# Kernel optimization log

Measured on AMD Instinct MI355X. Metric: run time of the kernel, lower is better.

The kernel has to match this reference:

```python
import jax, jax.numpy as jnp
import numpy as np

N, P = 512, 256
GAMMA = 1.0


def _linear_w(key, out_dim, in_dim):
    # torch nn.Linear default init: U(-1/sqrt(fan_in), 1/sqrt(fan_in))
    bound = 1.0 / np.sqrt(in_dim)
    return jax.random.uniform(key, (out_dim, in_dim), jnp.float32, -bound, bound)


def setup_inputs() -> dict:
    key = jax.random.key(0)
    ks = jax.random.split(key, 11)
    grad = jax.random.normal(ks[0], (N, P), jnp.float32)
    gradm1 = jax.random.normal(ks[1], (N, P), jnp.float32)
    dm1 = jax.random.normal(ks[2], (N, P), jnp.float32)
    # reset_mat(n_traj=N): identity per trajectory
    predicted_mat = jnp.broadcast_to(jnp.eye(P, dtype=jnp.float32), (N, P, P)).copy()
    return {
        "grad": grad, "gradm1": gradm1, "dm1": dm1, "predicted_mat": predicted_mat,
        "W_fullskip": _linear_w(ks[3], 1, 6),
        "Wo1": _linear_w(ks[4], 6, 3),
        "Wo2": _linear_w(ks[5], 12, 6),
        "Wo3": _linear_w(ks[6], 3, 12),
        "Wl1": _linear_w(ks[7], 12, 6),
        "Wl2": _linear_w(ks[8], 24, 12),
        "Wl3": _linear_w(ks[9], 1, 24),
    }


def reference(grad, gradm1, dm1, predicted_mat, W_fullskip, Wo1, Wo2, Wo3, Wl1, Wl2, Wl3):
    relu = jax.nn.relu
    # --- construct_features (torch.no_grad) ---
    QNDG = jnp.einsum('npq,nq->np', predicted_mat, grad - gradm1)          # (N,P)
    Bg = -GAMMA * jnp.einsum('npq,nq->np', predicted_mat, grad)            # (N,P)
    # cat along feature dim then reshape(N,3,P).transpose -> stack on last axis
    x = jnp.stack([QNDG, dm1, Bg], axis=-1)                                # (N,P,3)
    x = jax.lax.stop_gradient(x)
    # --- outer_FF: per-coordinate tiny MLP, then mean over P ---
    of = relu(x @ Wo1.T)
    of = relu(of @ Wo2.T)
    of = of @ Wo3.T                                                        # (N,P,3)
    of = jnp.mean(of, axis=1)                                              # (N,3)
    of = jnp.broadcast_to(of[:, None, :], x.shape)                         # (N,P,3)
    x6 = jnp.concatenate([x, of], axis=-1)                                 # (N,P,6)
    # --- full skip connection ---
    fullskip = (x6 @ W_fullskip.T)[..., 0]                                 # (N,P)
    # --- inner MLP (layers) ---
    out = relu(x6 @ Wl1.T)
    out = relu(out @ Wl2.T)
    out = (out @ Wl3.T)[..., 0]                                            # (N,P)
    out = out + fullskip
    # --- BFGS-like rank-2 update ---
    DGK = grad - gradm1                                                    # (N,P)
    secant = x[:, :, 1] - x[:, :, 0]                                       # dm1 - QNDG
    denom = jnp.sum(out * DGK, axis=-1, keepdims=True)                     # (N,1)
    normalization = (1.0 / denom)[:, :, None]                              # (N,1,1)
    coef = (jnp.sum(secant * DGK, axis=-1, keepdims=True) / denom)[:, :, None]
    upd = normalization * (
        secant[:, :, None] * out[:, None, :]
        + out[:, :, None] * secant[:, None, :]
        - coef * out[:, :, None] * out[:, None, :]
    )                                                                      # (N,P,P)
    new_mat = predicted_mat + upd
    v = -jax.lax.stop_gradient(grad)
    d = jnp.einsum('npq,nq->np', new_mat, v)                               # (N,P)
    return d
```

## Files before the change

### kernel.cpp

```cpp
#include <hip/hip_runtime.h>

#define NT 512
#define PD 256

__device__ __forceinline__ float wave_reduce_sum(float v) {
    #pragma unroll
    for (int m = 32; m >= 1; m >>= 1) v += __shfl_xor(v, m, 64);
    return v;
}

__global__ __launch_bounds__(256) void matvec2_kernel(
    const float* __restrict__ pm, const float* __restrict__ grad,
    const float* __restrict__ gradm1, float* __restrict__ qndg,
    float* __restrict__ pg)
{
    const int tid  = threadIdx.x;
    const int lane = tid & 63;
    const int wave = tid >> 6;
    const int n     = blockIdx.x >> 2;
    const int chunk = blockIdx.x & 3;

    const float4 g4  = ((const float4*)(grad   + n * PD))[lane];
    const float4 gm4 = ((const float4*)(gradm1 + n * PD))[lane];
    const float4 dg4 = make_float4(g4.x - gm4.x, g4.y - gm4.y,
                                   g4.z - gm4.z, g4.w - gm4.w);

    const int row0 = chunk * 64 + wave * 16;
    const float* base = pm + (size_t)n * PD * PD;
    #pragma unroll 4
    for (int r = 0; r < 16; ++r) {
        const int row = row0 + r;
        const float4 m4 = ((const float4*)(base + (size_t)row * PD))[lane];
        float aq = m4.x * dg4.x + m4.y * dg4.y + m4.z * dg4.z + m4.w * dg4.w;
        float ag = m4.x * g4.x  + m4.y * g4.y  + m4.z * g4.z  + m4.w * g4.w;
        aq = wave_reduce_sum(aq);
        ag = wave_reduce_sum(ag);
        if (lane == 0) {
            qndg[n * PD + row] = aq;
            pg[n * PD + row]   = ag;
        }
    }
}

__global__ __launch_bounds__(256) void epilogue_kernel(
    const float* __restrict__ qndg, const float* __restrict__ pgin,
    const float* __restrict__ grad, const float* __restrict__ gradm1,
    const float* __restrict__ dm1,
    const float* __restrict__ Wfs, const float* __restrict__ Wo1,
    const float* __restrict__ Wo2, const float* __restrict__ Wo3,
    const float* __restrict__ Wl1, const float* __restrict__ Wl2,
    const float* __restrict__ Wl3,
    float* __restrict__ dout)
{
    __shared__ float sW[516];
    __shared__ float redA[4][3];
    __shared__ float redB[4][4];

    const int tid  = threadIdx.x;
    const int lane = tid & 63;
    const int wave = tid >> 6;
    const int n    = blockIdx.x;

    if (tid < 18) sW[tid]       = Wo1[tid];
    if (tid < 72) sW[18 + tid]  = Wo2[tid];
    if (tid < 36) sW[90 + tid]  = Wo3[tid];
    if (tid < 72) sW[126 + tid] = Wl1[tid];
    sW[198 + tid] = Wl2[tid];
    if (tid < 32) sW[198 + 256 + tid] = Wl2[256 + tid];
    if (tid < 24) sW[486 + tid] = Wl3[tid];
    if (tid < 6)  sW[510 + tid] = Wfs[tid];
    __syncthreads();

    const int idx = n * PD + tid;
    const float q   = qndg[idx];
    const float bg  = -pgin[idx];
    const float g   = grad[idx];
    const float gm  = gradm1[idx];
    const float dm  = dm1[idx];

    const float x0 = q, x1 = dm, x2 = bg;

    float h1[6];
    #pragma unroll
    for (int j = 0; j < 6; ++j) {
        float s = sW[j*3] * x0 + sW[j*3 + 1] * x1 + sW[j*3 + 2] * x2;
        h1[j] = fmaxf(s, 0.f);
    }
    float h2[12];
    #pragma unroll
    for (int j = 0; j < 12; ++j) {
        float s = 0.f;
        #pragma unroll
        for (int i = 0; i < 6; ++i) s += sW[18 + j*6 + i] * h1[i];
        h2[j] = fmaxf(s, 0.f);
    }
    float o0 = 0.f, o1 = 0.f, o2 = 0.f;
    #pragma unroll
    for (int i = 0; i < 12; ++i) {
        o0 += sW[90 + i]      * h2[i];
        o1 += sW[90 + 12 + i] * h2[i];
        o2 += sW[90 + 24 + i] * h2[i];
    }

    float r0 = wave_reduce_sum(o0);
    float r1 = wave_reduce_sum(o1);
    float r2 = wave_reduce_sum(o2);
    if (lane == 0) { redA[wave][0] = r0; redA[wave][1] = r1; redA[wave][2] = r2; }
    __syncthreads();
    const float inv = 1.0f / 256.0f;
    const float of0 = (redA[0][0] + redA[1][0] + redA[2][0] + redA[3][0]) * inv;
    const float of1 = (redA[0][1] + redA[1][1] + redA[2][1] + redA[3][1]) * inv;
    const float of2 = (redA[0][2] + redA[1][2] + redA[2][2] + redA[3][2]) * inv;

    const float x6[6] = {x0, x1, x2, of0, of1, of2};

    float fullskip = 0.f;
    #pragma unroll
    for (int i = 0; i < 6; ++i) fullskip += sW[510 + i] * x6[i];

    float l1[12];
    #pragma unroll
    for (int j = 0; j < 12; ++j) {
        float s = 0.f;
        #pragma unroll
        for (int i = 0; i < 6; ++i) s += sW[126 + j*6 + i] * x6[i];
        l1[j] = fmaxf(s, 0.f);
    }
    float l2[24];
    #pragma unroll
    for (int j = 0; j < 24; ++j) {
        float s = 0.f;
        #pragma unroll
        for (int i = 0; i < 12; ++i) s += sW[198 + j*12 + i] * l1[i];
        l2[j] = fmaxf(s, 0.f);
    }
    float out = fullskip;
    #pragma unroll
    for (int i = 0; i < 24; ++i) out += sW[486 + i] * l2[i];

    const float dgk    = g - gm;
    const float secant = dm - q;

    float pd  = wave_reduce_sum(out * dgk);
    float ps  = wave_reduce_sum(secant * dgk);
    float po  = wave_reduce_sum(out * g);
    float psg = wave_reduce_sum(secant * g);
    if (lane == 0) {
        redB[wave][0] = pd; redB[wave][1] = ps;
        redB[wave][2] = po; redB[wave][3] = psg;
    }
    __syncthreads();
    const float denom = redB[0][0] + redB[1][0] + redB[2][0] + redB[3][0];
    const float sdgk  = redB[0][1] + redB[1][1] + redB[2][1] + redB[3][1];
    const float og    = redB[0][2] + redB[1][2] + redB[2][2] + redB[3][2];
    const float sg    = redB[0][3] + redB[1][3] + redB[2][3] + redB[3][3];

    const float invd = 1.0f / denom;
    const float coef = sdgk * invd;
    const float d = bg + (-secant * og - out * sg + coef * out * og) * invd;
    dout[idx] = d;
}

extern "C" void kernel_launch(void* const* d_in, const int* in_sizes, int n_in,
                              void* d_out, int out_size, void* d_ws, size_t ws_size,
                              hipStream_t stream) {
    const float* grad   = (const float*)d_in[0];
    const float* gradm1 = (const float*)d_in[1];
    const float* dm1    = (const float*)d_in[2];
    const float* pm     = (const float*)d_in[3];
    const float* Wfs    = (const float*)d_in[4];
    const float* Wo1    = (const float*)d_in[5];
    const float* Wo2    = (const float*)d_in[6];
    const float* Wo3    = (const float*)d_in[7];
    const float* Wl1    = (const float*)d_in[8];
    const float* Wl2    = (const float*)d_in[9];
    const float* Wl3    = (const float*)d_in[10];

    float* qndg = (float*)d_ws;
    float* pgbuf = qndg + NT * PD;

    matvec2_kernel<<<NT * 4, 256, 0, stream>>>(pm, grad, gradm1, qndg, pgbuf);
    epilogue_kernel<<<NT, 256, 0, stream>>>(qndg, pgbuf, grad, gradm1, dm1,
                                            Wfs, Wo1, Wo2, Wo3, Wl1, Wl2, Wl3,
                                            (float*)d_out);
}
```

Baseline: 221.3 us.

## Fuse matvec and MLP epilogue into one kernel with double-buffered LDS tiles

Merges the two-matrix-vector kernel and the MLP/BFGS epilogue into a single kernel with one block per trajectory. This removes the intermediate qndg/pg round trip through global memory and the second launch. The matrix is streamed in 32-row tiles through two padded LDS buffers, prefetching the next tile into registers while the current one is consumed. Each thread accumulates partial dot products over a 32-column slice, and the partials are reduced in LDS. The cost is far fewer blocks (512 instead of 2048 plus 512), heavy LDS use that limits occupancy, and a dynamic register-array index (gv[t&31]) that may spill to scratch.

Result: faster. 216.5 us (-2.2%).

```diff
diff --git a/kernel.cpp b/kernel.cpp
--- a/kernel.cpp
+++ b/kernel.cpp
@@ -2,6 +2,9 @@
 
 #define NT 512
 #define PD 256
+#define TROWS 32
+#define NTILES 8
+#define LPITCH 257
 
 __device__ __forceinline__ float wave_reduce_sum(float v) {
     #pragma unroll
@@ -9,74 +12,127 @@
     return v;
 }
 
-__global__ __launch_bounds__(256) void matvec2_kernel(
+__global__ __launch_bounds__(256) void fused_kernel(
     const float* __restrict__ pm, const float* __restrict__ grad,
-    const float* __restrict__ gradm1, float* __restrict__ qndg,
-    float* __restrict__ pg)
-{
-    const int tid  = threadIdx.x;
-    const int lane = tid & 63;
-    const int wave = tid >> 6;
-    const int n     = blockIdx.x >> 2;
-    const int chunk = blockIdx.x & 3;
-
-    const float4 g4  = ((const float4*)(grad   + n * PD))[lane];
-    const float4 gm4 = ((const float4*)(gradm1 + n * PD))[lane];
-    const float4 dg4 = make_float4(g4.x - gm4.x, g4.y - gm4.y,
-                                   g4.z - gm4.z, g4.w - gm4.w);
-
-    const int row0 = chunk * 64 + wave * 16;
-    const float* base = pm + (size_t)n * PD * PD;
-    #pragma unroll 4
-    for (int r = 0; r < 16; ++r) {
-        const int row = row0 + r;
-        const float4 m4 = ((const float4*)(base + (size_t)row * PD))[lane];
-        float aq = m4.x * dg4.x + m4.y * dg4.y + m4.z * dg4.z + m4.w * dg4.w;
-        float ag = m4.x * g4.x  + m4.y * g4.y  + m4.z * g4.z  + m4.w * g4.w;
-        aq = wave_reduce_sum(aq);
-        ag = wave_reduce_sum(ag);
-        if (lane == 0) {
-            qndg[n * PD + row] = aq;
-            pg[n * PD + row]   = ag;
-        }
-    }
-}
-
-__global__ __launch_bounds__(256) void epilogue_kernel(
-    const float* __restrict__ qndg, const float* __restrict__ pgin,
-    const float* __restrict__ grad, const float* __restrict__ gradm1,
-    const float* __restrict__ dm1,
+    const float* __restrict__ gradm1, const float* __restrict__ dm1,
     const float* __restrict__ Wfs, const float* __restrict__ Wo1,
     const float* __restrict__ Wo2, const float* __restrict__ Wo3,
     const float* __restrict__ Wl1, const float* __restrict__ Wl2,
-    const float* __restrict__ Wl3,
-    float* __restrict__ dout)
+    const float* __restrict__ Wl3, float* __restrict__ dout)
 {
+    __shared__ float buf0[TROWS * LPITCH];
+    __shared__ float buf1[TROWS * LPITCH];
     __shared__ float sW[516];
     __shared__ float redA[4][3];
     __shared__ float redB[4][4];
 
-    const int tid  = threadIdx.x;
-    const int lane = tid & 63;
-    const int wave = tid >> 6;
+    const int t    = threadIdx.x;
+    const int lane = t & 63;
+    const int wave = t >> 6;
     const int n    = blockIdx.x;
 
-    if (tid < 18) sW[tid]       = Wo1[tid];
-    if (tid < 72) sW[18 + tid]  = Wo2[tid];
-    if (tid < 36) sW[90 + tid]  = Wo3[tid];
-    if (tid < 72) sW[126 + tid] = Wl1[tid];
-    sW[198 + tid] = Wl2[tid];
-    if (tid < 32) sW[198 + 256 + tid] = Wl2[256 + tid];
-    if (tid < 24) sW[486 + tid] = Wl3[tid];
-    if (tid < 6)  sW[510 + tid] = Wfs[tid];
-    __syncthreads();
-
-    const int idx = n * PD + tid;
-    const float q   = qndg[idx];
-    const float bg  = -pgin[idx];
-    const float g   = grad[idx];
-    const float gm  = gradm1[idx];
-    const float dm  = dm1[idx];
+    if (t < 18) sW[t]       = Wo1[t];
+    if (t < 72) sW[18 + t]  = Wo2[t];
+    if (t < 36) sW[90 + t]  = Wo3[t];
+    if (t < 72) sW[126 + t] = Wl1[t];
+    sW[198 + t] = Wl2[t];
+    if (t < 32) sW[198 + 256 + t] = Wl2[256 + t];
+    if (t < 24) sW[486 + t] = Wl3[t];
+    if (t < 6)  sW[510 + t] = Wfs[t];
+
+    const int r  = t & 31;
+    const int cg = t >> 5;
+    float gv[32], dgv[32];
+    {
+        const float4* gb  = (const float4*)(grad   + n * PD + cg * 32);
+        const float4* gmb = (const float4*)(gradm1 + n * PD + cg * 32);
+        #pragma unroll
+        for (int i = 0; i < 8; ++i) {
+            float4 a = gb[i];
+            float4 b = gmb[i];
+            gv[4*i+0] = a.x; gv[4*i+1] = a.y; gv[4*i+2] = a.z; gv[4*i+3] = a.w;
+            dgv[4*i+0] = a.x - b.x; dgv[4*i+1] = a.y - b.y;
+            dgv[4*i+2] = a.z - b.z; dgv[4*i+3] = a.w - b.w;
+        }
+    }
+
+    const float* tbase = pm + (size_t)n * PD * PD;
+    float4 stg[8];
+    float accq[NTILES], accg[NTILES];
+
+
+    #pragma unroll
+    for (int j = 0; j < 8; ++j) {
+        const int row = 4 * j + wave;
+        stg[j] = ((const float4*)(tbase + (size_t)(0 * TROWS + row) * PD))[lane];
+    }
+    #pragma unroll
+    for (int j = 0; j < 8; ++j) {
+        const int row = 4 * j + wave;
+        float* p = buf0 + row * LPITCH + lane;
+        p[0] = stg[j].x; p[64] = stg[j].y; p[128] = stg[j].z; p[192] = stg[j].w;
+    }
+    __syncthreads();
+
+    #pragma unroll
+    for (int k = 0; k < NTILES; ++k) {
+        if (k + 1 < NTILES) {
+            #pragma unroll
+            for (int j = 0; j < 8; ++j) {
+                const int row = 4 * j + wave;
+                stg[j] = ((const float4*)(tbase + (size_t)((k + 1) * TROWS + row) * PD))[lane];
+            }
+        }
+        {
+            const float* bp = ((k & 1) ? buf1 : buf0) + r * LPITCH + 8 * cg;
+            float sq = 0.f, sg = 0.f;
+            #pragma unroll
+            for (int p = 0; p < 4; ++p) {
+                #pragma unroll
+                for (int q = 0; q < 8; ++q) {
+                    const float m = bp[p * 64 + q];
+                    sq += m * dgv[4*q + p];
+                    sg += m * gv[4*q + p];
+                }
+            }
+            accq[k] = sq; accg[k] = sg;
+        }
+        if (k + 1 < NTILES) {
+            float* wb = ((k + 1) & 1) ? buf1 : buf0;
+            #pragma unroll
+            for (int j = 0; j < 8; ++j) {
+                const int row = 4 * j + wave;
+                float* p = wb + row * LPITCH + lane;
+                p[0] = stg[j].x; p[64] = stg[j].y; p[128] = stg[j].z; p[192] = stg[j].w;
+            }
+        }
+        __syncthreads();
+    }
+
+    float* partsQ = buf0;
+    float* partsG = buf0 + 2048;
+    #pragma unroll
+    for (int k = 0; k < NTILES; ++k) {
+        partsQ[k * 256 + t] = accq[k];
+        partsG[k * 256 + t] = accg[k];
+    }
+    __syncthreads();
+
+    float q = 0.f, pg = 0.f;
+    {
+        const int pb = (t >> 5) * 256 + (t & 31);
+        #pragma unroll
+        for (int c = 0; c < 8; ++c) {
+            q  += partsQ[pb + 32 * c];
+            pg += partsG[pb + 32 * c];
+        }
+    }
+
+    const int idx = n * PD + t;
+    const float bg = -pg;
+    const float g  = gv[t & 31];
+    const float gm = g - dgv[t & 31];
+    const float dm = dm1[idx];
 
     const float x0 = q, x1 = dm, x2 = bg;
 
@@ -153,11 +209,11 @@
     const float denom = redB[0][0] + redB[1][0] + redB[2][0] + redB[3][0];
     const float sdgk  = redB[0][1] + redB[1][1] + redB[2][1] + redB[3][1];
     const float og    = redB[0][2] + redB[1][2] + redB[2][2] + redB[3][2];
-    const float sg    = redB[0][3] + redB[1][3] + redB[2][3] + redB[3][3];
+    const float sg2   = redB[0][3] + redB[1][3] + redB[2][3] + redB[3][3];
 
     const float invd = 1.0f / denom;
     const float coef = sdgk * invd;
-    const float d = bg + (-secant * og - out * sg + coef * out * og) * invd;
+    const float d = bg + (-secant * og - out * sg2 + coef * out * og) * invd;
     dout[idx] = d;
 }
 
@@ -176,11 +232,7 @@
     const float* Wl2    = (const float*)d_in[9];
     const float* Wl3    = (const float*)d_in[10];
 
-    float* qndg = (float*)d_ws;
-    float* pgbuf = qndg + NT * PD;
-
-    matvec2_kernel<<<NT * 4, 256, 0, stream>>>(pm, grad, gradm1, qndg, pgbuf);
-    epilogue_kernel<<<NT, 256, 0, stream>>>(qndg, pgbuf, grad, gradm1, dm1,
-                                            Wfs, Wo1, Wo2, Wo3, Wl1, Wl2, Wl3,
-                                            (float*)d_out);
+    fused_kernel<<<NT, 256, 0, stream>>>(pm, grad, gradm1, dm1,
+                                         Wfs, Wo1, Wo2, Wo3, Wl1, Wl2, Wl3,
+                                         (float*)d_out);
 }
```
